# Kernel tuning notes

Hardware: AMD Instinct MI355X
Metric: run time of the kernel (lower is better)

The kernel has to match this reference:

```python
import jax, jax.numpy as jnp
import numpy as np

B, C, H, W = 8, 512, 64, 64
K = 8
NUM = K * K          # number of channel groups / graph nodes
CG = C // NUM        # channels per group (8)
NC = 19              # num_classes
OUT = 512            # bottleneck out_channels


def make_dct_weight():
    # Per-channel 2D DCT basis. Channel ch belongs to group g = ch // CG;
    # group g selects frequency (u, v) = (g % K, g // K).
    g = np.arange(C) // CG
    u = (g % K).astype(np.float64)
    v = (g // K).astype(np.float64)
    th = (np.arange(H) + 0.5) / H   # [H]
    tw = (np.arange(W) + 0.5) / W   # [W]
    bh = np.cos(np.pi * u[:, None] * th[None, :])  # [C,H]
    bw = np.cos(np.pi * v[:, None] * tw[None, :])  # [C,W]
    return (bh[:, :, None] * bw[:, None, :]).astype(np.float32)  # [C,H,W]


def setup_inputs() -> dict:
    key = jax.random.key(0)
    ks = jax.random.split(key, 10)
    s = lambda i, shape: jax.random.normal(ks[i], shape, jnp.float32) * 0.05
    return {
        'x': jax.random.normal(ks[0], (B, C, H, W), jnp.float32),
        'dct_w': jnp.asarray(make_dct_weight()),
        'dm_w1': s(1, (CG, CG)),
        'dm_gamma': jnp.ones((CG,), jnp.float32),
        'dm_beta': jnp.zeros((CG,), jnp.float32),
        'dm_w2': s(2, (NC, CG)),
        'dm_b2': s(3, (NC,)),
        'fuse_w': s(4, (NUM,)),
        'fuse_b': s(5, (1,)),
        'gcn_w1': s(6, (NUM, NUM)),
        'gcn_w2': s(7, (CG, CG)),
        'bot_w': s(8, (OUT, 2 * C, 3, 3)),
        'bot_gamma': jnp.ones((OUT,), jnp.float32),
        'bot_beta': jnp.zeros((OUT,), jnp.float32),
    }


def reference(x, dct_w, dm_w1, dm_gamma, dm_beta, dm_w2, dm_b2,
              fuse_w, fuse_b, gcn_w1, gcn_w2, bot_w, bot_gamma, bot_beta):
    # MultiSpectralDCTLayer: elementwise DCT basis multiply, keeps [B,C,H,W]
    fres = x * dct_w[None]

    # channel_split -> grouped layout [B, NUM, CG, H*W]
    xg = x.reshape(B, NUM, CG, H * W)
    fg = fres.reshape(B, NUM, CG, H * W)

    # decoder_map: 1x1 conv -> BN(eval, mean=0,var=1) -> ReLU -> (Dropout=id) -> 1x1 conv
    h1 = jnp.einsum('dc,bncp->bndp', dm_w1, fg)
    h1 = jax.nn.relu(h1 * dm_gamma[None, None, :, None] + dm_beta[None, None, :, None])
    fres_map = jnp.einsum('kc,bncp->bnkp', dm_w2, h1) + dm_b2[None, None, :, None]  # [B,n,NC,HW]

    # fuse: 1x1 conv over group dim n -> [B,NC,H,W]
    fres_map_output = (jnp.einsum('n,bnkp->bkp', fuse_w, fres_map) + fuse_b[0]).reshape(B, NC, H, W)

    # local frequency class centers: [B,n,NC,HW] @ [B,n,HW,c] -> [B,n,NC,c]
    fHWc = fg.transpose(0, 1, 3, 2)   # [B,n,HW,c]
    xHWc = xg.transpose(0, 1, 3, 2)   # [B,n,HW,c]
    local = jnp.einsum('bnkp,bnpc->bnkc', fres_map, fHWc)

    # GCN over n (node) dim: conv1 + residual ReLU, then Linear over c
    g = jnp.einsum('mn,bnkc->bmkc', gcn_w1, local)
    g = jax.nn.relu(g + local)
    local = jnp.einsum('bnkc,dc->bnkd', g, gcn_w2)

    # attention combine: softmax(x @ local^T) @ local
    wm = jax.nn.softmax(jnp.einsum('bnpc,bnkc->bnpk', xHWc, local), axis=-1)  # [B,n,HW,NC]
    out = jnp.einsum('bnpk,bnkc->bnpc', wm, local)  # [B,n,HW,c]

    # channel_recover -> [B,C,H,W]
    out = out.transpose(0, 1, 3, 2).reshape(B, C, H, W)

    # bottleneck: 3x3 conv on concat, BN(eval) affine, ReLU
    cat = jnp.concatenate([x, out], axis=1)  # [B,2C,H,W]
    y = jax.lax.conv_general_dilated(cat, bot_w, (1, 1), 'SAME',
                                     dimension_numbers=('NCHW', 'OIHW', 'NCHW'))
    y = jax.nn.relu(y * bot_gamma[None, :, None, None] + bot_beta[None, :, None, None])
    return (y, fres_map_output)
```

## Files before the change

kernel.cpp:

```cpp
#include <hip/hip_runtime.h>


typedef __attribute__((ext_vector_type(8))) unsigned short u16x8;
typedef __attribute__((ext_vector_type(8))) __bf16 bf16x8;
typedef __attribute__((ext_vector_type(4))) float f32x4;

__device__ inline unsigned short f2bf(float f) {
    unsigned int u = __float_as_uint(f);
    u += 0x7fffu + ((u >> 16) & 1u);
    return (unsigned short)(u >> 16);
}

__device__ __forceinline__ void gload16(unsigned short* lds, const unsigned short* g) {
    __builtin_amdgcn_global_load_lds(
        (const __attribute__((address_space(1))) unsigned int*)g,
        (__attribute__((address_space(3))) unsigned int*)lds, 16, 0, 0);
}

__global__ __launch_bounds__(256) void repack_w(const float* __restrict__ w,
                                                unsigned short* __restrict__ wt) {
    __shared__ float buf[9216];
    const int oc = blockIdx.x;
    const int tid = threadIdx.x;
    const float* src = w + (size_t)oc * 9216;
    for (int i = tid; i < 9216; i += 256) buf[i] = src[i];
    __syncthreads();
#pragma unroll
    for (int t = 0; t < 9; ++t) {
        for (int i = tid; i < 1024; i += 256)
            wt[((size_t)t * 512 + oc) * 1024 + i] = f2bf(buf[i * 9 + t]);
    }
}

__global__ __launch_bounds__(256) void front_kernel(
    const float* __restrict__ x, const float* __restrict__ dct,
    const float* __restrict__ w1, const float* __restrict__ gamma,
    const float* __restrict__ beta, const float* __restrict__ w2,
    const float* __restrict__ b2, const float* __restrict__ fuse_w,
    float* __restrict__ part, float* __restrict__ fpart,
    unsigned short* __restrict__ cat) {
    __shared__ __align__(16) float fgs[8][260];
    __shared__ __align__(16) float fms[19][260];
    __shared__ float sw1[64], sw2[152], sb2[19], sg[8], sb[8], sfw[64];
    const int bid = blockIdx.x;
    const int sp = bid >> 7;
    const int b = (bid >> 4) & 7;
    const int ch = bid & 15;
    const int tid = threadIdx.x;
    if (tid < 64) { sw1[tid] = w1[tid]; sfw[tid] = fuse_w[tid]; }
    if (tid < 152) sw2[tid] = w2[tid];
    if (tid < 19) sb2[tid] = b2[tid];
    if (tid < 8) { sg[tid] = gamma[tid]; sb[tid] = beta[tid]; }
    __syncthreads();
    const int p = ch * 256 + tid;
    const int kk = tid >> 3, cc = tid & 7;
    float facc[19];
#pragma unroll
    for (int k = 0; k < 19; ++k) facc[k] = 0.f;
    for (int nn = 0; nn < 16; ++nn) {
        const int n = sp * 16 + nn;
        float fg[8];
        u16x8 xw;
#pragma unroll
        for (int c = 0; c < 8; ++c) {
            const float xv = x[((size_t)(b * 512 + n * 8 + c)) * 4096 + p];
            fg[c] = xv * dct[((size_t)(n * 8 + c)) * 4096 + p];
            xw[c] = f2bf(xv);
            fgs[c][tid] = fg[c];
        }
        *(u16x8*)(cat + ((size_t)(b * 4096) + p) * 1024 + n * 8) = xw;
        float h1[8];
#pragma unroll
        for (int d = 0; d < 8; ++d) {
            float s = 0.f;
#pragma unroll
            for (int c = 0; c < 8; ++c) s = fmaf(sw1[d * 8 + c], fg[c], s);
            h1[d] = fmaxf(fmaf(s, sg[d], sb[d]), 0.f);
        }
        const float fw = sfw[n];
#pragma unroll
        for (int k = 0; k < 19; ++k) {
            float s = sb2[k];
#pragma unroll
            for (int d = 0; d < 8; ++d) s = fmaf(sw2[k * 8 + d], h1[d], s);
            fms[k][tid] = s;
            facc[k] = fmaf(fw, s, facc[k]);
        }
        __syncthreads();
        if (tid < 152) {
            float accv = 0.f;
#pragma unroll 8
            for (int p4 = 0; p4 < 256; p4 += 4) {
                const float4 a = *(const float4*)&fms[kk][p4];
                const float4 g4 = *(const float4*)&fgs[cc][p4];
                accv += a.x * g4.x + a.y * g4.y + a.z * g4.z + a.w * g4.w;
            }
            part[((size_t)((b * 64 + n) * 16) + ch) * 152 + tid] = accv;
        }
        __syncthreads();
    }
#pragma unroll
    for (int k = 0; k < 19; ++k)
        fpart[((size_t)(sp * 8 + b) * 19 + k) * 4096 + p] = facc[k];
}

__global__ __launch_bounds__(256) void fuse_reduce(
    const float* __restrict__ fpart, const float* __restrict__ fuse_b,
    float* __restrict__ out1) {
    const int i = blockIdx.x * 256 + threadIdx.x;
    float s = fuse_b[0];
#pragma unroll
    for (int sp = 0; sp < 4; ++sp) s += fpart[(size_t)sp * 622592 + i];
    out1[i] = s;
}

__global__ __launch_bounds__(256) void gcn_kernel(
    const float* __restrict__ part, const float* __restrict__ w1,
    const float* __restrict__ w2, float* __restrict__ local2) {
    __shared__ float L[9728];
    __shared__ float R[9728];
    __shared__ float sw1[4096];
    __shared__ float sw2[64];
    const int b = blockIdx.x;
    const int tid = threadIdx.x;
    for (int i = tid; i < 4096; i += 256) sw1[i] = w1[i];
    if (tid < 64) sw2[tid] = w2[tid];
    for (int i = tid; i < 9728; i += 256) {
        int n = i / 152, t = i - n * 152;
        float s = 0.f;
#pragma unroll
        for (int ch = 0; ch < 16; ++ch)
            s += part[((size_t)((b * 64 + n) * 16) + ch) * 152 + t];
        L[i] = s;
    }
    __syncthreads();
    for (int i = tid; i < 9728; i += 256) {
        int m = i / 152, t = i - m * 152;
        float g = 0.f;
        for (int n = 0; n < 64; ++n) g = fmaf(sw1[m * 64 + n], L[n * 152 + t], g);
        R[i] = fmaxf(g + L[i], 0.f);
    }
    __syncthreads();
    for (int i = tid; i < 9728; i += 256) {
        int n = i / 152, t = i - n * 152;
        int k = t >> 3, d = t & 7;
        float s = 0.f;
#pragma unroll
        for (int c = 0; c < 8; ++c) s = fmaf(R[n * 152 + k * 8 + c], sw2[d * 8 + c], s);
        local2[(size_t)b * 9728 + i] = s;
    }
}

__global__ __launch_bounds__(256) void attn_kernel(
    const float* __restrict__ x, const float* __restrict__ local2,
    unsigned short* __restrict__ cat) {
    __shared__ float L[152];
    const int bn = blockIdx.x;
    const int b = bn >> 6, n = bn & 63;
    const int tid = threadIdx.x;
    if (tid < 152) L[tid] = local2[(size_t)bn * 152 + tid];
    __syncthreads();
    for (int i = 0; i < 16; ++i) {
        const int p = i * 256 + tid;
        float xv[8];
#pragma unroll
        for (int c = 0; c < 8; ++c)
            xv[c] = x[((size_t)(b * 512 + n * 8 + c)) * 4096 + p];
        float lg[19];
        float mx = -1e30f;
#pragma unroll
        for (int k = 0; k < 19; ++k) {
            float s = 0.f;
#pragma unroll
            for (int c = 0; c < 8; ++c) s = fmaf(xv[c], L[k * 8 + c], s);
            lg[k] = s;
            mx = fmaxf(mx, s);
        }
        float se = 0.f;
#pragma unroll
        for (int k = 0; k < 19; ++k) {
            lg[k] = __expf(lg[k] - mx);
            se += lg[k];
        }
        const float inv = 1.f / se;
        float ov[8];
#pragma unroll
        for (int c = 0; c < 8; ++c) ov[c] = 0.f;
#pragma unroll
        for (int k = 0; k < 19; ++k) {
#pragma unroll
            for (int c = 0; c < 8; ++c) ov[c] = fmaf(lg[k], L[k * 8 + c], ov[c]);
        }
        u16x8 w;
#pragma unroll
        for (int c = 0; c < 8; ++c) w[c] = f2bf(ov[c] * inv);
        *(u16x8*)(cat + ((size_t)(b * 4096) + p) * 1024 + 512 + n * 8) = w;
    }
}

__global__ __launch_bounds__(512, 1) void conv_kernel(
    const unsigned short* __restrict__ cat, const unsigned short* __restrict__ wt,
    const unsigned short* __restrict__ zp,
    const float* __restrict__ gamma, const float* __restrict__ beta,
    float* __restrict__ out) {
    __shared__ __align__(16) unsigned short As[10 * 4096];
    __shared__ __align__(16) unsigned short Bs[2 * 16384];
    const int bid0 = blockIdx.x;
    const int bid = (bid0 & 7) * 32 + (bid0 >> 3);
    const int mt = bid >> 1;
    const int nt = bid & 1;
    const int b = mt >> 4;
    const int pix0 = (mt & 15) * 256;
    const int y0 = (mt & 15) * 4;
    const int ocb = nt * 256;
    const int tid = threadIdx.x;
    const int w = tid >> 6;
    const int lane = tid & 63;
    const int l16 = lane & 15;
    const int khalf = lane >> 4;
    const int wr1 = w >> 2;
    const int wrow = wr1 * 64;
    const int wcol = (w & 3) * 32;
    const int sx = tid >> 3;
    const int icsw = ((tid & 7) ^ ((tid >> 3) & 7)) * 8;
    const unsigned short* zps = zp + icsw;
    const unsigned short* catb = cat + ((size_t)b * 4096) * 1024 + icsw;
    int colk[3][2];
#pragma unroll
    for (int d = 0; d < 3; ++d)
#pragma unroll
        for (int ks = 0; ks < 2; ++ks)
            colk[d][ks] = ((ks * 64 + khalf * 16) ^ (((l16 + d - 1) & 7) << 4)) >> 1;

    f32x4 acc[2][2][4][2];
#pragma unroll
    for (int qm = 0; qm < 2; ++qm)
#pragma unroll
        for (int qn = 0; qn < 2; ++qn)
#pragma unroll
            for (int m = 0; m < 4; ++m)
#pragma unroll
                for (int n = 0; n < 2; ++n)
#pragma unroll
                    for (int j = 0; j < 4; ++j) acc[qm][qn][m][n][j] = 0.f;

    bf16x8 af[4][2];
    bf16x8 bq[2][2];
    const bf16x8 zf = {};

#define AF_READ(QM, DY, DX)                                                        \
    {                                                                              \
        const int r_ = (QM) * 2 + wr1 + (DY) + 1;                                  \
        const int phys_ = (r_ < 2) ? r_ : r_ + 4 * cp;                             \
        const int rb_ = phys_ * 4096;                                              \
        _Pragma("unroll") for (int m_ = 0; m_ < 4; ++m_) {                         \
            const int xm_ = m_ * 16 + l16 + (DX);                                  \
            const int xc_ = ((DX) == 0) ? xm_ : min(max(xm_, 0), 63);              \
            const int ab_ = rb_ + xc_ * 64;                                        \
            _Pragma("unroll") for (int ks_ = 0; ks_ < 2; ++ks_)                    \
                af[m_][ks_] = *(const bf16x8*)(As + ab_ + colk[(DX) + 1][ks_]);    \
            if ((DX) == -1 && m_ == 0 && l16 == 0) { af[0][0] = zf; af[0][1] = zf; } \
            if ((DX) == 1 && m_ == 3 && l16 == 15) { af[3][0] = zf; af[3][1] = zf; } \
        }                                                                          \
    }

#define BQ_READ(SOFF, QN)                                                          \
    _Pragma("unroll") for (int n_ = 0; n_ < 2; ++n_)                               \
        _Pragma("unroll") for (int ks_ = 0; ks_ < 2; ++ks_)                        \
            bq[n_][ks_] = *(const bf16x8*)(Bs + (SOFF) +                           \
                ((QN) * 128 + wcol + n_ * 16 + l16) * 64 + colk[1][ks_]);

#define STAGE_BH(H, SWOFF, TAP, ICB)                                               \
    _Pragma("unroll") for (int j_ = 0; j_ < 2; ++j_) {                             \
        gload16(Bs + (SWOFF) + (H) * 8192 + (j_ * 512 + tid) * 8,                  \
                wt + (size_t)(TAP) * 524288 +                                      \
                    (size_t)(ocb + (H) * 128 + j_ * 64 + sx) * 1024 + (ICB) + icsw); \
    }

#define STAGE_AROW(R)                                                              \
    do {                                                                           \
        const int yy_ = y0 - 1 + (R);                                              \
        const int ph_ = ((R) < 2) ? (R) : (R) + 4 * cp1;                           \
        const unsigned short* s2_ = ((unsigned)yy_ < 64u)                          \
            ? catb + ((size_t)(yy_ * 64 + sx)) * 1024 + iccn : zps;                \
        gload16(As + ph_ * 4096 + tid * 8, s2_);                                   \
    } while (0)

#define MFMA16(QM, QN)                                                             \
    __builtin_amdgcn_s_setprio(1);                                                 \
    _Pragma("unroll") for (int m_ = 0; m_ < 4; ++m_)                               \
        _Pragma("unroll") for (int n_ = 0; n_ < 2; ++n_)                           \
            _Pragma("unroll") for (int ks_ = 0; ks_ < 2; ++ks_)                    \
                acc[QM][QN][m_][n_] = __builtin_amdgcn_mfma_f32_16x16x32_bf16(     \
                    af[m_][ks_], bq[n_][ks_], acc[QM][QN][m_][n_], 0, 0, 0);       \
    __builtin_amdgcn_s_setprio(0);

#define VWAIT(N)                                                                   \
    asm volatile("s_waitcnt vmcnt(" #N ")" ::: "memory");                          \
    __builtin_amdgcn_sched_barrier(0);

#define TAP_BODY(T, DY, DX, AROW, W0N, W2N)                                        \
    {                                                                              \
        const int s_ = (c + (T)) & 1;                                              \
        const int sr_ = s_ << 14;                                                  \
        const int sw_ = sr_ ^ 16384;                                               \
        const int tn_ = ((T) == 8) ? 0 : (T) + 1;                                  \
        const int icb_ = ((T) == 8) ? iccn : icc;                                  \
                                                                 \
        VWAIT(W0N)                                                                 \
        __builtin_amdgcn_s_barrier();                                              \
        __builtin_amdgcn_sched_barrier(0);                                         \
        AF_READ(0, DY, DX)                                                         \
        BQ_READ(sr_, 0)                                                            \
        STAGE_BH(0, sw_, tn_, icb_)                                                \
        MFMA16(0, 0)                                                               \
                                                                 \
        AF_READ(1, DY, DX)                                                         \
        if ((AROW) >= 0) STAGE_AROW(AROW);                                         \
        MFMA16(1, 0)                                                               \
                                                                 \
        VWAIT(W2N)                                                                 \
        BQ_READ(sr_, 1)                                                            \
        STAGE_BH(1, sw_, tn_, icb_)                                                \
        MFMA16(1, 1)                                                               \
                                                                 \
        AF_READ(0, DY, DX)                                                         \
        MFMA16(0, 1)                                                               \
    }

    {
        const int cp1 = 0, iccn = 0;
#pragma unroll
        for (int r = 0; r < 6; ++r) STAGE_AROW(r);
    }
    STAGE_BH(0, 0, 0, 0)
    STAGE_BH(1, 0, 0, 0)

    for (int c = 0; c < 16; ++c) {
        const int cp = c & 1;
        const int cp1 = cp ^ 1;
        const int icc = c << 6;
        const int iccn = ((c + 1) & 15) << 6;
        TAP_BODY(0, -1, -1, -1, 2, 2)
        TAP_BODY(1, -1, 0, -1, 2, 2)
        TAP_BODY(2, -1, 1, -1, 2, 2)
        TAP_BODY(3, 0, -1, 0, 2, 3)
        TAP_BODY(4, 0, 0, 2, 3, 3)
        TAP_BODY(5, 0, 1, 3, 3, 3)
        TAP_BODY(6, 1, -1, 1, 3, 3)
        TAP_BODY(7, 1, 0, 4, 3, 3)
        TAP_BODY(8, 1, 1, 5, 3, 3)
    }
    asm volatile("s_waitcnt vmcnt(0)" ::: "memory");

#pragma unroll
    for (int qn = 0; qn < 2; ++qn)
#pragma unroll
        for (int n = 0; n < 2; ++n) {
            const int oc = ocb + qn * 128 + wcol + n * 16 + l16;
            const float g = gamma[oc], bb = beta[oc];
#pragma unroll
            for (int qm = 0; qm < 2; ++qm)
#pragma unroll
                for (int m = 0; m < 4; ++m) {
                    const int P = qm * 128 + wrow + m * 16 + khalf * 4;
                    float4 o;
                    o.x = fmaxf(fmaf(acc[qm][qn][m][n][0], g, bb), 0.f);
                    o.y = fmaxf(fmaf(acc[qm][qn][m][n][1], g, bb), 0.f);
                    o.z = fmaxf(fmaf(acc[qm][qn][m][n][2], g, bb), 0.f);
                    o.w = fmaxf(fmaf(acc[qm][qn][m][n][3], g, bb), 0.f);
                    *(float4*)(out + ((size_t)(b * 512 + oc)) * 4096 + pix0 + P) = o;
                }
        }
#undef AF_READ
#undef BQ_READ
#undef STAGE_BH
#undef STAGE_AROW
#undef MFMA16
#undef VWAIT
#undef TAP_BODY
}

extern "C" void kernel_launch(void* const* d_in, const int* in_sizes, int n_in,
                              void* d_out, int out_size, void* d_ws, size_t ws_size,
                              hipStream_t stream) {
    const float* x = (const float*)d_in[0];
    const float* dct = (const float*)d_in[1];
    const float* dm_w1 = (const float*)d_in[2];
    const float* dm_g = (const float*)d_in[3];
    const float* dm_b = (const float*)d_in[4];
    const float* dm_w2 = (const float*)d_in[5];
    const float* dm_b2 = (const float*)d_in[6];
    const float* fuse_w = (const float*)d_in[7];
    const float* fuse_b = (const float*)d_in[8];
    const float* gcn_w1 = (const float*)d_in[9];
    const float* gcn_w2 = (const float*)d_in[10];
    const float* bot_w = (const float*)d_in[11];
    const float* bot_g = (const float*)d_in[12];
    const float* bot_b = (const float*)d_in[13];

    float* y = (float*)d_out;
    float* out1 = y + (size_t)8 * 512 * 4096;
    float* part = y;
    float* fpart = y + 1245184;

    char* ws = (char*)d_ws;
    const size_t CAT_BYTES = (size_t)8 * 4096 * 1024 * 2;
    const size_t WT_BYTES = (size_t)9 * 512 * 1024 * 2;
    const size_t PART_BYTES = (size_t)2048 * 152 * 4;
    const size_t L2_BYTES = (size_t)8 * 9728 * 4;
    const size_t ZP_BYTES = 4096;
    if (ws_size < CAT_BYTES + WT_BYTES + PART_BYTES + L2_BYTES + ZP_BYTES) return;

    unsigned short* cat = (unsigned short*)ws;
    unsigned short* wt = (unsigned short*)(ws + CAT_BYTES);
    float* local2 = (float*)(ws + CAT_BYTES + WT_BYTES + PART_BYTES);
    unsigned short* zp = (unsigned short*)(ws + CAT_BYTES + WT_BYTES + PART_BYTES + L2_BYTES);

    hipMemsetAsync(zp, 0, ZP_BYTES, stream);
    front_kernel<<<dim3(512), dim3(256), 0, stream>>>(x, dct, dm_w1, dm_g, dm_b,
                                                      dm_w2, dm_b2, fuse_w,
                                                      part, fpart, cat);
    fuse_reduce<<<dim3(2432), dim3(256), 0, stream>>>(fpart, fuse_b, out1);
    gcn_kernel<<<dim3(8), dim3(256), 0, stream>>>(part, gcn_w1, gcn_w2, local2);
    repack_w<<<dim3(512), dim3(256), 0, stream>>>(bot_w, wt);
    attn_kernel<<<dim3(512), dim3(256), 0, stream>>>(x, local2, cat);
    conv_kernel<<<dim3(256), dim3(512), 0, stream>>>(cat, wt, zp, bot_g, bot_b, y);
}
```

Baseline: 410.1 us.

## Switch conv MFMA from 16x16x32 to 32x32x16 tiles with reworked fragment loads

Replaces the 16x16x32 bf16 MFMA tiling in the 3x3 conv implicit GEMM with 32x32x16 instructions. Each wave now covers 4 row tiles by 2 column tiles of 32x32, with new swizzled LDS addressing and border zeroing for the shifted taps. The larger tiles cut LDS fragment reads per FLOP, so A is no longer re-read within a tap. The cost is a different register footprint and a new epilogue output mapping.

```diff
diff --git a/kernel.cpp b/kernel.cpp
--- a/kernel.cpp
+++ b/kernel.cpp
@@ -4,6 +4,7 @@
 typedef __attribute__((ext_vector_type(8))) unsigned short u16x8;
 typedef __attribute__((ext_vector_type(8))) __bf16 bf16x8;
 typedef __attribute__((ext_vector_type(4))) float f32x4;
+typedef __attribute__((ext_vector_type(16))) float f32x16;
 
 __device__ inline unsigned short f2bf(float f) {
     unsigned int u = __float_as_uint(f);
@@ -216,59 +217,54 @@
     const int tid = threadIdx.x;
     const int w = tid >> 6;
     const int lane = tid & 63;
-    const int l16 = lane & 15;
-    const int khalf = lane >> 4;
+    const int l31 = lane & 31;
+    const int hk = lane >> 5;
     const int wr1 = w >> 2;
-    const int wrow = wr1 * 64;
-    const int wcol = (w & 3) * 32;
+    const int wc32 = (w & 3) * 32;
     const int sx = tid >> 3;
     const int icsw = ((tid & 7) ^ ((tid >> 3) & 7)) * 8;
     const unsigned short* zps = zp + icsw;
     const unsigned short* catb = cat + ((size_t)b * 4096) * 1024 + icsw;
-    int colk[3][2];
-#pragma unroll
-    for (int d = 0; d < 3; ++d)
-#pragma unroll
-        for (int ks = 0; ks < 2; ++ks)
-            colk[d][ks] = ((ks * 64 + khalf * 16) ^ (((l16 + d - 1) & 7) << 4)) >> 1;
-
-    f32x4 acc[2][2][4][2];
-#pragma unroll
-    for (int qm = 0; qm < 2; ++qm)
-#pragma unroll
-        for (int qn = 0; qn < 2; ++qn)
-#pragma unroll
-            for (int m = 0; m < 4; ++m)
-#pragma unroll
-                for (int n = 0; n < 2; ++n)
-#pragma unroll
-                    for (int j = 0; j < 4; ++j) acc[qm][qn][m][n][j] = 0.f;
-
-    bf16x8 af[4][2];
-    bf16x8 bq[2][2];
+    int kcol[4];
+#pragma unroll
+    for (int ks = 0; ks < 4; ++ks) kcol[ks] = ks * 16 + hk * 8;
+    int keyd[3];
+#pragma unroll
+    for (int d = 0; d < 3; ++d) keyd[d] = ((l31 + d - 1) & 7) << 3;
+    const int keyb = (l31 & 7) << 3;
+
+    f32x16 acc[4][2];
+#pragma unroll
+    for (int rt = 0; rt < 4; ++rt)
+#pragma unroll
+        for (int ct = 0; ct < 2; ++ct)
+#pragma unroll
+            for (int j = 0; j < 16; ++j) acc[rt][ct][j] = 0.f;
+
+    bf16x8 afr[2][2][4];
+    bf16x8 bq[2];
     const bf16x8 zf = {};
 
-#define AF_READ(QM, DY, DX)                                                        \
-    {                                                                              \
-        const int r_ = (QM) * 2 + wr1 + (DY) + 1;                                  \
+#define AF_PAIR(PAIR, DY, DX, DXI)                                                 \
+    _Pragma("unroll") for (int rt_ = 0; rt_ < 4; ++rt_) {                          \
+        const int r_ = wr1 * 2 + (rt_ >> 1) + (DY) + 1;                            \
         const int phys_ = (r_ < 2) ? r_ : r_ + 4 * cp;                             \
-        const int rb_ = phys_ * 4096;                                              \
-        _Pragma("unroll") for (int m_ = 0; m_ < 4; ++m_) {                         \
-            const int xm_ = m_ * 16 + l16 + (DX);                                  \
-            const int xc_ = ((DX) == 0) ? xm_ : min(max(xm_, 0), 63);              \
-            const int ab_ = rb_ + xc_ * 64;                                        \
-            _Pragma("unroll") for (int ks_ = 0; ks_ < 2; ++ks_)                    \
-                af[m_][ks_] = *(const bf16x8*)(As + ab_ + colk[(DX) + 1][ks_]);    \
-            if ((DX) == -1 && m_ == 0 && l16 == 0) { af[0][0] = zf; af[0][1] = zf; } \
-            if ((DX) == 1 && m_ == 3 && l16 == 15) { af[3][0] = zf; af[3][1] = zf; } \
-        }                                                                          \
-    }
-
-#define BQ_READ(SOFF, QN)                                                          \
-    _Pragma("unroll") for (int n_ = 0; n_ < 2; ++n_)                               \
-        _Pragma("unroll") for (int ks_ = 0; ks_ < 2; ++ks_)                        \
-            bq[n_][ks_] = *(const bf16x8*)(Bs + (SOFF) +                           \
-                ((QN) * 128 + wcol + n_ * 16 + l16) * 64 + colk[1][ks_]);
+        int x_ = (rt_ & 1) * 32 + l31 + (DX);                                      \
+        if ((DX) != 0) x_ = min(max(x_, 0), 63);                                   \
+        const int ab_ = phys_ * 4096 + x_ * 64;                                    \
+        _Pragma("unroll") for (int kk_ = 0; kk_ < 2; ++kk_)                        \
+            afr[PAIR][kk_][rt_] = *(const bf16x8*)(As + ab_ +                      \
+                (kcol[(PAIR) * 2 + kk_] ^ keyd[DXI]));                             \
+        if ((DX) == -1 && (rt_ & 1) == 0 && l31 == 0) {                            \
+            afr[PAIR][0][rt_] = zf; afr[PAIR][1][rt_] = zf; }                      \
+        if ((DX) == 1 && (rt_ & 1) == 1 && l31 == 31) {                            \
+            afr[PAIR][0][rt_] = zf; afr[PAIR][1][rt_] = zf; }                      \
+    }
+
+#define BQ_PAIR(SR, CT, PAIR)                                                      \
+    _Pragma("unroll") for (int kk_ = 0; kk_ < 2; ++kk_)                            \
+        bq[kk_] = *(const bf16x8*)(Bs + (SR) +                                     \
+            ((CT) * 128 + wc32 + l31) * 64 + (kcol[(PAIR) * 2 + kk_] ^ keyb));
 
 #define STAGE_BH(H, SWOFF, TAP, ICB)                                               \
     _Pragma("unroll") for (int j_ = 0; j_ < 2; ++j_) {                             \
@@ -286,46 +282,46 @@
         gload16(As + ph_ * 4096 + tid * 8, s2_);                                   \
     } while (0)
 
-#define MFMA16(QM, QN)                                                             \
+#define MFMA8(PAIR, CT)                                                            \
     __builtin_amdgcn_s_setprio(1);                                                 \
-    _Pragma("unroll") for (int m_ = 0; m_ < 4; ++m_)                               \
-        _Pragma("unroll") for (int n_ = 0; n_ < 2; ++n_)                           \
-            _Pragma("unroll") for (int ks_ = 0; ks_ < 2; ++ks_)                    \
-                acc[QM][QN][m_][n_] = __builtin_amdgcn_mfma_f32_16x16x32_bf16(     \
-                    af[m_][ks_], bq[n_][ks_], acc[QM][QN][m_][n_], 0, 0, 0);       \
+    _Pragma("unroll") for (int kk_ = 0; kk_ < 2; ++kk_)                            \
+        _Pragma("unroll") for (int rt_ = 0; rt_ < 4; ++rt_)                        \
+            acc[rt_][CT] = __builtin_amdgcn_mfma_f32_32x32x16_bf16(                \
+                afr[PAIR][kk_][rt_], bq[kk_], acc[rt_][CT], 0, 0, 0);              \
     __builtin_amdgcn_s_setprio(0);
 
 #define VWAIT(N)                                                                   \
     asm volatile("s_waitcnt vmcnt(" #N ")" ::: "memory");                          \
     __builtin_amdgcn_sched_barrier(0);
 
-#define TAP_BODY(T, DY, DX, AROW, W0N, W2N)                                        \
+#define TAP_BODY(T, DY, DX, DXI, AROW, W0N, W2N)                                   \
     {                                                                              \
         const int s_ = (c + (T)) & 1;                                              \
         const int sr_ = s_ << 14;                                                  \
         const int sw_ = sr_ ^ 16384;                                               \
         const int tn_ = ((T) == 8) ? 0 : (T) + 1;                                  \
         const int icb_ = ((T) == 8) ? iccn : icc;                                  \
-                                                                 \
+                                                          \
         VWAIT(W0N)                                                                 \
         __builtin_amdgcn_s_barrier();                                              \
         __builtin_amdgcn_sched_barrier(0);                                         \
-        AF_READ(0, DY, DX)                                                         \
-        BQ_READ(sr_, 0)                                                            \
+        AF_PAIR(0, DY, DX, DXI)                                                    \
+        BQ_PAIR(sr_, 0, 0)                                                         \
         STAGE_BH(0, sw_, tn_, icb_)                                                \
-        MFMA16(0, 0)                                                               \
-                                                                 \
-        AF_READ(1, DY, DX)                                                         \
+        MFMA8(0, 0)                                                                \
+                                                          \
+        AF_PAIR(1, DY, DX, DXI)                                                    \
+        BQ_PAIR(sr_, 0, 1)                                                         \
         if ((AROW) >= 0) STAGE_AROW(AROW);                                         \
-        MFMA16(1, 0)                                                               \
-                                                                 \
+        MFMA8(1, 0)                                                                \
+                                                          \
         VWAIT(W2N)                                                                 \
-        BQ_READ(sr_, 1)                                                            \
+        BQ_PAIR(sr_, 1, 0)                                                         \
         STAGE_BH(1, sw_, tn_, icb_)                                                \
-        MFMA16(1, 1)                                                               \
-                                                                 \
-        AF_READ(0, DY, DX)                                                         \
-        MFMA16(0, 1)                                                               \
+        MFMA8(0, 1)                                                                \
+                                                          \
+        BQ_PAIR(sr_, 1, 1)                                                         \
+        MFMA8(1, 1)                                                                \
     }
 
     {
@@ -341,42 +337,42 @@
         const int cp1 = cp ^ 1;
         const int icc = c << 6;
         const int iccn = ((c + 1) & 15) << 6;
-        TAP_BODY(0, -1, -1, -1, 2, 2)
-        TAP_BODY(1, -1, 0, -1, 2, 2)
-        TAP_BODY(2, -1, 1, -1, 2, 2)
-        TAP_BODY(3, 0, -1, 0, 2, 3)
-        TAP_BODY(4, 0, 0, 2, 3, 3)
-        TAP_BODY(5, 0, 1, 3, 3, 3)
-        TAP_BODY(6, 1, -1, 1, 3, 3)
-        TAP_BODY(7, 1, 0, 4, 3, 3)
-        TAP_BODY(8, 1, 1, 5, 3, 3)
+        TAP_BODY(0, -1, -1, 0, -1, 2, 2)
+        TAP_BODY(1, -1, 0, 1, -1, 2, 2)
+        TAP_BODY(2, -1, 1, 2, -1, 2, 2)
+        TAP_BODY(3, 0, -1, 0, 0, 2, 3)
+        TAP_BODY(4, 0, 0, 1, 2, 3, 3)
+        TAP_BODY(5, 0, 1, 2, 3, 3, 3)
+        TAP_BODY(6, 1, -1, 0, 1, 3, 3)
+        TAP_BODY(7, 1, 0, 1, 4, 3, 3)
+        TAP_BODY(8, 1, 1, 2, 5, 3, 3)
     }
     asm volatile("s_waitcnt vmcnt(0)" ::: "memory");
 
 #pragma unroll
-    for (int qn = 0; qn < 2; ++qn)
-#pragma unroll
-        for (int n = 0; n < 2; ++n) {
-            const int oc = ocb + qn * 128 + wcol + n * 16 + l16;
+    for (int rt = 0; rt < 4; ++rt) {
+        const int pxb = pix0 + (wr1 * 2 + (rt >> 1)) * 64 + (rt & 1) * 32 + hk * 4;
+#pragma unroll
+        for (int ct = 0; ct < 2; ++ct) {
+            const int oc = ocb + ct * 128 + wc32 + l31;
             const float g = gamma[oc], bb = beta[oc];
-#pragma unroll
-            for (int qm = 0; qm < 2; ++qm)
-#pragma unroll
-                for (int m = 0; m < 4; ++m) {
-                    const int P = qm * 128 + wrow + m * 16 + khalf * 4;
-                    float4 o;
-                    o.x = fmaxf(fmaf(acc[qm][qn][m][n][0], g, bb), 0.f);
-                    o.y = fmaxf(fmaf(acc[qm][qn][m][n][1], g, bb), 0.f);
-                    o.z = fmaxf(fmaf(acc[qm][qn][m][n][2], g, bb), 0.f);
-                    o.w = fmaxf(fmaf(acc[qm][qn][m][n][3], g, bb), 0.f);
-                    *(float4*)(out + ((size_t)(b * 512 + oc)) * 4096 + pix0 + P) = o;
-                }
-        }
-#undef AF_READ
-#undef BQ_READ
+            float* op = out + ((size_t)(b * 512 + oc)) * 4096 + pxb;
+#pragma unroll
+            for (int g2 = 0; g2 < 4; ++g2) {
+                float4 o;
+                o.x = fmaxf(fmaf(acc[rt][ct][g2 * 4 + 0], g, bb), 0.f);
+                o.y = fmaxf(fmaf(acc[rt][ct][g2 * 4 + 1], g, bb), 0.f);
+                o.z = fmaxf(fmaf(acc[rt][ct][g2 * 4 + 2], g, bb), 0.f);
+                o.w = fmaxf(fmaf(acc[rt][ct][g2 * 4 + 3], g, bb), 0.f);
+                *(float4*)(op + g2 * 8) = o;
+            }
+        }
+    }
+#undef AF_PAIR
+#undef BQ_PAIR
 #undef STAGE_BH
 #undef STAGE_AROW
-#undef MFMA16
+#undef MFMA8
 #undef VWAIT
 #undef TAP_BODY
 }
```

Measured after the change: 469.8 us. 1.15x slower.

## Split GCN across more blocks and keep both A-fragment sets in registers

Applied to the files above, without the earlier changes.

The single 8-block GCN kernel becomes two kernels. One is a wide reduction kernel that sums the partial local-center tiles into a global buffer. The other is a 64-block GCN kernel where each block handles 8 nodes, so the node mixing runs across many more CUs instead of 8. In the conv kernel, the two A-fragment register sets (qm=0 and qm=1) are now kept live, which removes the repeated AF_READ of the qm=0 fragments before the last MFMA quarter in every tap. The trade-off is higher VGPR pressure in the conv kernel plus an extra launch and round trip through global memory for the reduction.

```diff
diff --git a/kernel.cpp b/kernel.cpp
--- a/kernel.cpp
+++ b/kernel.cpp
@@ -114,40 +114,47 @@
     out1[i] = s;
 }
 
-__global__ __launch_bounds__(256) void gcn_kernel(
-    const float* __restrict__ part, const float* __restrict__ w1,
+__global__ __launch_bounds__(256) void lsum_kernel(
+    const float* __restrict__ part, float* __restrict__ L) {
+    const int i = blockIdx.x * 256 + threadIdx.x;
+    const int bn = i / 152;
+    const int t = i - bn * 152;
+    float s = 0.f;
+#pragma unroll
+    for (int ch = 0; ch < 16; ++ch)
+        s += part[((size_t)(bn * 16 + ch)) * 152 + t];
+    L[i] = s;
+}
+
+__global__ __launch_bounds__(256) void gcn2_kernel(
+    const float* __restrict__ Lg, const float* __restrict__ w1,
     const float* __restrict__ w2, float* __restrict__ local2) {
     __shared__ float L[9728];
-    __shared__ float R[9728];
+    __shared__ float R[1216];
     __shared__ float sw1[4096];
     __shared__ float sw2[64];
-    const int b = blockIdx.x;
+    const int b = blockIdx.x >> 3;
+    const int n0 = (blockIdx.x & 7) * 8;
     const int tid = threadIdx.x;
+    for (int i = tid; i < 9728; i += 256) L[i] = Lg[(size_t)b * 9728 + i];
     for (int i = tid; i < 4096; i += 256) sw1[i] = w1[i];
     if (tid < 64) sw2[tid] = w2[tid];
-    for (int i = tid; i < 9728; i += 256) {
-        int n = i / 152, t = i - n * 152;
-        float s = 0.f;
-#pragma unroll
-        for (int ch = 0; ch < 16; ++ch)
-            s += part[((size_t)((b * 64 + n) * 16) + ch) * 152 + t];
-        L[i] = s;
-    }
     __syncthreads();
-    for (int i = tid; i < 9728; i += 256) {
-        int m = i / 152, t = i - m * 152;
+    for (int i = tid; i < 1216; i += 256) {
+        const int nn = i / 152, t = i - nn * 152;
+        const int m = n0 + nn;
         float g = 0.f;
         for (int n = 0; n < 64; ++n) g = fmaf(sw1[m * 64 + n], L[n * 152 + t], g);
-        R[i] = fmaxf(g + L[i], 0.f);
+        R[i] = fmaxf(g + L[m * 152 + t], 0.f);
     }
     __syncthreads();
-    for (int i = tid; i < 9728; i += 256) {
-        int n = i / 152, t = i - n * 152;
-        int k = t >> 3, d = t & 7;
+    for (int i = tid; i < 1216; i += 256) {
+        const int nn = i / 152, t = i - nn * 152;
+        const int k = t >> 3, d = t & 7;
         float s = 0.f;
 #pragma unroll
-        for (int c = 0; c < 8; ++c) s = fmaf(R[n * 152 + k * 8 + c], sw2[d * 8 + c], s);
-        local2[(size_t)b * 9728 + i] = s;
+        for (int c = 0; c < 8; ++c) s = fmaf(R[nn * 152 + k * 8 + c], sw2[d * 8 + c], s);
+        local2[(size_t)b * 9728 + (n0 + nn) * 152 + t] = s;
     }
 }
 
@@ -244,11 +251,12 @@
 #pragma unroll
                     for (int j = 0; j < 4; ++j) acc[qm][qn][m][n][j] = 0.f;
 
-    bf16x8 af[4][2];
+    bf16x8 af0[4][2];
+    bf16x8 af1[4][2];
     bf16x8 bq[2][2];
     const bf16x8 zf = {};
 
-#define AF_READ(QM, DY, DX)                                                        \
+#define AF_READ(AFD, QM, DY, DX)                                                   \
     {                                                                              \
         const int r_ = (QM) * 2 + wr1 + (DY) + 1;                                  \
         const int phys_ = (r_ < 2) ? r_ : r_ + 4 * cp;                             \
@@ -258,9 +266,9 @@
             const int xc_ = ((DX) == 0) ? xm_ : min(max(xm_, 0), 63);              \
             const int ab_ = rb_ + xc_ * 64;                                        \
             _Pragma("unroll") for (int ks_ = 0; ks_ < 2; ++ks_)                    \
-                af[m_][ks_] = *(const bf16x8*)(As + ab_ + colk[(DX) + 1][ks_]);    \
-            if ((DX) == -1 && m_ == 0 && l16 == 0) { af[0][0] = zf; af[0][1] = zf; } \
-            if ((DX) == 1 && m_ == 3 && l16 == 15) { af[3][0] = zf; af[3][1] = zf; } \
+                AFD[m_][ks_] = *(const bf16x8*)(As + ab_ + colk[(DX) + 1][ks_]);   \
+            if ((DX) == -1 && m_ == 0 && l16 == 0) { AFD[0][0] = zf; AFD[0][1] = zf; } \
+            if ((DX) == 1 && m_ == 3 && l16 == 15) { AFD[3][0] = zf; AFD[3][1] = zf; } \
         }                                                                          \
     }
 
@@ -286,13 +294,13 @@
         gload16(As + ph_ * 4096 + tid * 8, s2_);                                   \
     } while (0)
 
-#define MFMA16(QM, QN)                                                             \
+#define MFMA_Q(AFD, QM, QN)                                                        \
     __builtin_amdgcn_s_setprio(1);                                                 \
     _Pragma("unroll") for (int m_ = 0; m_ < 4; ++m_)                               \
         _Pragma("unroll") for (int n_ = 0; n_ < 2; ++n_)                           \
             _Pragma("unroll") for (int ks_ = 0; ks_ < 2; ++ks_)                    \
                 acc[QM][QN][m_][n_] = __builtin_amdgcn_mfma_f32_16x16x32_bf16(     \
-                    af[m_][ks_], bq[n_][ks_], acc[QM][QN][m_][n_], 0, 0, 0);       \
+                    AFD[m_][ks_], bq[n_][ks_], acc[QM][QN][m_][n_], 0, 0, 0);      \
     __builtin_amdgcn_s_setprio(0);
 
 #define VWAIT(N)                                                                   \
@@ -306,26 +314,25 @@
         const int sw_ = sr_ ^ 16384;                                               \
         const int tn_ = ((T) == 8) ? 0 : (T) + 1;                                  \
         const int icb_ = ((T) == 8) ? iccn : icc;                                  \
-                                                                 \
+                                                                  \
         VWAIT(W0N)                                                                 \
         __builtin_amdgcn_s_barrier();                                              \
         __builtin_amdgcn_sched_barrier(0);                                         \
-        AF_READ(0, DY, DX)                                                         \
+        AF_READ(af0, 0, DY, DX)                                                    \
         BQ_READ(sr_, 0)                                                            \
         STAGE_BH(0, sw_, tn_, icb_)                                                \
-        MFMA16(0, 0)                                                               \
-                                                                 \
-        AF_READ(1, DY, DX)                                                         \
+        MFMA_Q(af0, 0, 0)                                                          \
+                                                                  \
+        AF_READ(af1, 1, DY, DX)                                                    \
         if ((AROW) >= 0) STAGE_AROW(AROW);                                         \
-        MFMA16(1, 0)                                                               \
-                                                                 \
+        MFMA_Q(af1, 1, 0)                                                          \
+                                                                  \
         VWAIT(W2N)                                                                 \
         BQ_READ(sr_, 1)                                                            \
         STAGE_BH(1, sw_, tn_, icb_)                                                \
-        MFMA16(1, 1)                                                               \
-                                                                 \
-        AF_READ(0, DY, DX)                                                         \
-        MFMA16(0, 1)                                                               \
+        MFMA_Q(af1, 1, 1)                                                          \
+                                             \
+        MFMA_Q(af0, 0, 1)                                                          \
     }
 
     {
@@ -376,7 +383,7 @@
 #undef BQ_READ
 #undef STAGE_BH
 #undef STAGE_AROW
-#undef MFMA16
+#undef MFMA_Q
 #undef VWAIT
 #undef TAP_BODY
 }
@@ -403,6 +410,7 @@
     float* out1 = y + (size_t)8 * 512 * 4096;
     float* part = y;
     float* fpart = y + 1245184;
+    float* Lbuf = y + 3735552;
 
     char* ws = (char*)d_ws;
     const size_t CAT_BYTES = (size_t)8 * 4096 * 1024 * 2;
@@ -421,8 +429,9 @@
     front_kernel<<<dim3(512), dim3(256), 0, stream>>>(x, dct, dm_w1, dm_g, dm_b,
                                                       dm_w2, dm_b2, fuse_w,
                                                       part, fpart, cat);
+    lsum_kernel<<<dim3(304), dim3(256), 0, stream>>>(part, Lbuf);
+    gcn2_kernel<<<dim3(64), dim3(256), 0, stream>>>(Lbuf, gcn_w1, gcn_w2, local2);
     fuse_reduce<<<dim3(2432), dim3(256), 0, stream>>>(fpart, fuse_b, out1);
-    gcn_kernel<<<dim3(8), dim3(256), 0, stream>>>(part, gcn_w1, gcn_w2, local2);
     repack_w<<<dim3(512), dim3(256), 0, stream>>>(bot_w, wt);
     attn_kernel<<<dim3(512), dim3(256), 0, stream>>>(x, local2, cat);
     conv_kernel<<<dim3(256), dim3(512), 0, stream>>>(cat, wt, zp, bot_g, bot_b, y);
```

After: 396.1 us. -3.4%, faster.
